# Kernel tuning notes

Hardware: AMD Instinct MI355X
Metric: run time of the kernel (lower is better)

The kernel has to match this reference:

```python
import jax, jax.numpy as jnp
import numpy as np

L = 256  # grayscale_levels
THRESH = (50.0, 150.0)
BASE = (30, 80, 150)
INCR = (10, 15, 25)


def setup_inputs() -> dict:
    key = jax.random.key(0)
    image = jax.random.uniform(key, (8, 3, 1024, 1024), dtype=jnp.float32)
    return {"image": image}


def _glcm_contrast(gray_idx):
    # gray_idx: [H, W] int32 in [0, L). distance=1, angle=0 -> horizontal neighbor pairs.
    p1 = gray_idx[:, :-1].ravel()
    p2 = gray_idx[:, 1:].ravel()
    # 256x256 co-occurrence histogram via flattened scatter-add
    hist = jnp.zeros(L * L, jnp.float32).at[p1 * L + p2].add(1.0)
    hist = hist / jnp.float32(p1.size)
    lv = jnp.arange(L, dtype=jnp.float32)
    diff2 = (lv[:, None] - lv[None, :]) ** 2
    return jnp.sum(hist.reshape(L, L) * diff2)


def _grid_labels(H, W, n_segments):
    # Deterministic grid superpixels (stand-in for skimage SLIC's initial grid;
    # same downstream math: fill each segment with its region mean).
    gr = max(1, int(round(np.sqrt(n_segments * H / W))))
    gc = max(1, int(np.ceil(n_segments / gr)))
    r = (np.arange(H) * gr) // H
    c = (np.arange(W) * gc) // W
    labels = r[:, None] * gc + c[None, :]
    return jnp.asarray(labels, dtype=jnp.int32), gr * gc


def _region_mean_saliency(gray, labels, nseg):
    flat = labels.ravel()
    sums = jax.ops.segment_sum(gray.ravel(), flat, num_segments=nseg)
    cnts = jax.ops.segment_sum(jnp.ones_like(gray).ravel(), flat, num_segments=nseg)
    return (sums / jnp.maximum(cnts, 1.0))[labels]


def reference(image):
    B, C, H, W = image.shape
    gray = 0.299 * image[:, 0] + 0.587 * image[:, 1] + 0.114 * image[:, 2]
    gidx = jnp.clip((gray * (L - 1)).astype(jnp.int32), 0, L - 1)
    complexity = jax.vmap(_glcm_contrast)(gidx)  # [B]

    comp_np = np.asarray(jax.device_get(complexity))
    cluster_sets = []
    for cv in comp_np:
        tier = 0 if cv < THRESH[0] else (1 if cv < THRESH[1] else 2)
        k, d = BASE[tier], INCR[tier]
        cluster_sets.append([k - d, k, k + d])

    # region mean uses np.mean over all channels of the region -> channel-mean image
    chan_mean = image.mean(axis=1)  # [B, H, W]
    label_cache = {}
    sal_rows = []
    for i, cset in enumerate(cluster_sets):
        maps = []
        for n in cset:
            if n not in label_cache:
                label_cache[n] = _grid_labels(H, W, n)
            labels, nseg = label_cache[n]
            maps.append(_region_mean_saliency(chan_mean[i], labels, nseg))
        sal_rows.append(jnp.stack(maps))  # [3, H, W]
    saliency = jnp.stack(sal_rows)  # [B, 3, H, W]
    return saliency, complexity, jnp.asarray(cluster_sets, dtype=jnp.int32)
```

## Files before the change

### kernel.cpp

```cpp
#include <hip/hip_runtime.h>
#include <math.h>

#define HW 1024
#define PLANE (1024 * 1024)

typedef float vf4 __attribute__((ext_vector_type(4)));

__constant__ int GCS[8]   = {5, 6, 7, 9, 10, 12, 13, 14};
__constant__ int BBASE[8] = {0, 6, 13, 21, 31, 42, 55, 69};
__constant__ int GR9c[9]      = {4, 5, 6, 8, 9, 10, 11, 12, 13};
__constant__ int GC9c[9]      = {5, 6, 7, 9, 9, 10, 12, 13, 14};
__constant__ int GBASE9c[9]   = {0, 20, 50, 92, 164, 245, 345, 477, 633};
__constant__ int COLBASE9c[9] = {0, 5, 11, 18, 18, 27, 37, 49, 62};


__device__ __forceinline__ int wave_reduce_int(int v) {
#pragma unroll
    for (int off = 32; off > 0; off >>= 1) v += __shfl_down(v, off, 64);
    return v;
}

__global__ __launch_bounds__(256) void k_main(const float* __restrict__ img,
                                              float* __restrict__ partials,
                                              float* __restrict__ rowrec) {
    const int b = blockIdx.y;
    const int tid = threadIdx.x;
    const int lane = tid & 63;
    const int w = tid >> 6;
    const int row = (blockIdx.x << 2) + w;

    const float* p = img + (size_t)b * (3 * PLANE) + row * HW;

    __shared__ float cmS[4][1024];
    __shared__ float PS[4][260];
    __shared__ float BS[4][88];
    __shared__ int swred[4];

    vf4 R[4], G[4], Bv[4];
#pragma unroll
    for (int j = 0; j < 4; ++j) {
        const int c = ((j << 6) + lane) << 2;
        R[j] = __builtin_nontemporal_load((const vf4*)(p + c));
        G[j] = __builtin_nontemporal_load((const vf4*)(p + PLANE + c));
        Bv[j] = __builtin_nontemporal_load((const vf4*)(p + 2 * PLANE + c));
    }

    int acc = 0;
    int pend = 0;
    float csum[4];

#pragma unroll
    for (int j = 0; j < 4; ++j) {
        const int c = ((j << 6) + lane) << 2;

        const float m0 = (R[j].x + G[j].x + Bv[j].x) * (1.0f / 3.0f);
        const float m1 = (R[j].y + G[j].y + Bv[j].y) * (1.0f / 3.0f);
        const float m2 = (R[j].z + G[j].z + Bv[j].z) * (1.0f / 3.0f);
        const float m3 = (R[j].w + G[j].w + Bv[j].w) * (1.0f / 3.0f);
        *(float4*)&cmS[w][c] = make_float4(m0, m1, m2, m3);
        csum[j] = (m0 + m1) + (m2 + m3);

        const float g0 = 0.299f * R[j].x + 0.587f * G[j].x + 0.114f * Bv[j].x;
        const float g1 = 0.299f * R[j].y + 0.587f * G[j].y + 0.114f * Bv[j].y;
        const float g2 = 0.299f * R[j].z + 0.587f * G[j].z + 0.114f * Bv[j].z;
        const float g3 = 0.299f * R[j].w + 0.587f * G[j].w + 0.114f * Bv[j].w;

        const int gi0 = min(max((int)(g0 * 255.0f), 0), 255);
        const int gi1 = min(max((int)(g1 * 255.0f), 0), 255);
        const int gi2 = min(max((int)(g2 * 255.0f), 0), 255);
        const int gi3 = min(max((int)(g3 * 255.0f), 0), 255);

        const int first0 = __shfl(gi0, 0, 64);
        if (j > 0 && lane == 63) {
            const int d = pend - first0;
            acc += d * d;
        }
        const int nxt = __shfl_down(gi0, 1, 64);
        const int d0 = gi0 - gi1, d1 = gi1 - gi2, d2 = gi2 - gi3;
        acc += d0 * d0 + d1 * d1 + d2 * d2;
        if (lane != 63) {
            const int d = gi3 - nxt;
            acc += d * d;
        }
        pend = gi3;
    }

    float pre = 0.0f;
#pragma unroll
    for (int j = 0; j < 4; ++j) {
        float x = csum[j];
#pragma unroll
        for (int off = 1; off < 64; off <<= 1) {
            const float y = __shfl_up(x, off, 64);
            if (lane >= off) x += y;
        }
        PS[w][(j << 6) + lane] = pre + (x - csum[j]);
        pre += __shfl(x, 63, 64);
    }
    if (lane == 0) PS[w][256] = pre;

#pragma unroll
    for (int rep = 0; rep < 2; ++rep) {
        const int bnd = lane + (rep << 6);
        if (bnd < 84) {
            const int sct = (bnd >= 6) + (bnd >= 13) + (bnd >= 21) + (bnd >= 31) +
                            (bnd >= 42) + (bnd >= 55) + (bnd >= 69);
            const int gc = GCS[sct];
            const int i = bnd - BBASE[sct];
            const int c = (i * 1024 + gc - 1) / gc;
            const int m = c & 3;
            const int cb = min(c & ~3, 1020);
            float Bp = PS[w][c >> 2];
            const float a0 = cmS[w][cb], a1 = cmS[w][cb + 1], a2 = cmS[w][cb + 2];
            if (m > 0) Bp += a0;
            if (m > 1) Bp += a1;
            if (m > 2) Bp += a2;
            BS[w][bnd] = Bp;
        }
    }

    float* rr = rowrec + (size_t)((b << 10) + row) * 80;
#pragma unroll
    for (int rep = 0; rep < 2; ++rep) {
        const int k = lane + (rep << 6);
        if (k < 76) {
            const int sct = (k >= 5) + (k >= 11) + (k >= 18) + (k >= 27) +
                            (k >= 37) + (k >= 49) + (k >= 62);
            const int bidx = k + sct;
            rr[k] = BS[w][bidx + 1] - BS[w][bidx];
        }
    }

    acc = wave_reduce_int(acc);
    if (lane == 0) swred[w] = acc;
    __syncthreads();
    if (tid == 0)
        partials[(b << 8) + blockIdx.x] = (float)(swred[0] + swred[1] + swred[2] + swred[3]);
}

__global__ __launch_bounds__(256) void k_reduce(const float* __restrict__ rowrec,
                                                const float* __restrict__ partials,
                                                float* __restrict__ cellmean,
                                                float* __restrict__ out,
                                                int* __restrict__ tier_ws) {
    const int rc = blockIdx.x, g = blockIdx.y, b = blockIdx.z;
    const int t = threadIdx.x;
    const int gr = GR9c[g];
    const bool active = (rc < gr);

    __shared__ float red[16][17];
    __shared__ float compLDS[8];

    const int gc = GC9c[g];
    const int cb = COLBASE9c[g];
    const int r0 = (rc * 1024 + gr - 1) / gr;
    const int r1 = ((rc + 1) * 1024 + gr - 1) / gr;
    const int cc = t & 15, rch = t >> 4;

    if (active) {
        float s = 0.0f;
        if (cc < gc)
            for (int r = r0 + rch; r < r1; r += 16)
                s += rowrec[(size_t)((b << 10) + r) * 80 + cb + cc];
        red[rch][cc] = s;
    }

    const bool special = (rc == 0 && g == 0 && b == 0);
    if (special) {
        const int b2 = t >> 5, sub = t & 31;
        float sC = 0.0f;
#pragma unroll
        for (int kk = 0; kk < 8; ++kk) sC += partials[(b2 << 8) + sub + (kk << 5)];
#pragma unroll
        for (int off = 16; off > 0; off >>= 1) sC += __shfl_down(sC, off, 32);
        if (sub == 0) compLDS[b2] = sC;
    }

    __syncthreads();

    if (active && rch == 0 && cc < gc) {
        float tot = 0.0f;
#pragma unroll
        for (int q = 0; q < 16; ++q) tot += red[q][cc];
        const int c0 = (cc * 1024 + gc - 1) / gc;
        const int c1 = ((cc + 1) * 1024 + gc - 1) / gc;
        const float area = (float)((r1 - r0) * (c1 - c0));
        cellmean[b * 815 + GBASE9c[g] + rc * gc + cc] = tot / area;
    }

    if (special && t < 8) {
        const size_t OFFC = (size_t)8 * 3 * PLANE;
        const float cv = compLDS[t] * (1.0f / (1024.0f * 1023.0f));
        out[OFFC + t] = cv;
        const int tier = (cv < 50.0f) ? 0 : ((cv < 150.0f) ? 1 : 2);
        const int kk = (tier == 0) ? 30 : ((tier == 1) ? 80 : 150);
        const int dd = (tier == 0) ? 10 : ((tier == 1) ? 15 : 25);
#pragma unroll
        for (int j = 0; j < 3; ++j)
            out[OFFC + 8 + t * 3 + j] = (float)(kk + (j - 1) * dd);
        tier_ws[t] = tier;
    }
}

__global__ __launch_bounds__(256) void k_fill(const int* __restrict__ tier_ws,
                                              const float* __restrict__ cellmean,
                                              float* __restrict__ out) {
    const int jm = blockIdx.y, b = blockIdx.z;
    const int tid = threadIdx.x;
    const int g = tier_ws[b] * 3 + jm;
    const int gr = GR9c[g], gc = GC9c[g];
    const float* cmb = cellmean + b * 815 + GBASE9c[g];
    float* ob = out + ((size_t)(b * 3 + jm) << 20);
    const int col = tid << 2;
    const int i0 = (col * gc) >> 10, i1 = ((col + 1) * gc) >> 10;
    const int i2 = ((col + 2) * gc) >> 10, i3 = ((col + 3) * gc) >> 10;

#pragma unroll
    for (int i = 0; i < 4; ++i) {
        const int row = (blockIdx.x << 2) + i;
        const int rc = (row * gr) >> 10;
        const float* cm = cmb + rc * gc;
        vf4 o;
        o.x = cm[i0];
        o.y = cm[i1];
        o.z = cm[i2];
        o.w = cm[i3];
        __builtin_nontemporal_store(o, (vf4*)(ob + row * HW + col));
    }
}

extern "C" void kernel_launch(void* const* d_in, const int* in_sizes, int n_in,
                              void* d_out, int out_size, void* d_ws, size_t ws_size,
                              hipStream_t stream) {
    const float* img = (const float*)d_in[0];
    float* out = (float*)d_out;
    float* ws = (float*)d_ws;

    float* partials = ws;
    int* tier_ws = (int*)(ws + 2048);
    float* cellmean = ws + 2080;
    float* rowrec = ws + 16384;

    k_main<<<dim3(256, 8), 256, 0, stream>>>(img, partials, rowrec);
    k_reduce<<<dim3(13, 9, 8), 256, 0, stream>>>(rowrec, partials, cellmean, out, tier_ws);
    k_fill<<<dim3(256, 3, 8), 256, 0, stream>>>(tier_ws, cellmean, out);
}
```

Measured before the change: 46.25 us.

## Fuse reduce and fill kernels, recomputing cell means per block in LDS

Removes the separate k_reduce launch. Each fill block now recomputes the complexity tier from partials and sums the rowrec entries for the one or two cell rows it touches, keeping the cell means in LDS before writing its output rows. This drops one kernel launch and the global round trip for cellmean and tier, at the cost of redundant partial and rowrec reads in each of the 6144 blocks plus extra barriers.

```diff
diff --git a/kernel.cpp b/kernel.cpp
--- a/kernel.cpp
+++ b/kernel.cpp
@@ -10,11 +10,15 @@
 __constant__ int BBASE[8] = {0, 6, 13, 21, 31, 42, 55, 69};
 __constant__ int GR9c[9]      = {4, 5, 6, 8, 9, 10, 11, 12, 13};
 __constant__ int GC9c[9]      = {5, 6, 7, 9, 9, 10, 12, 13, 14};
-__constant__ int GBASE9c[9]   = {0, 20, 50, 92, 164, 245, 345, 477, 633};
 __constant__ int COLBASE9c[9] = {0, 5, 11, 18, 18, 27, 37, 49, 62};
 
 
 __device__ __forceinline__ int wave_reduce_int(int v) {
+#pragma unroll
+    for (int off = 32; off > 0; off >>= 1) v += __shfl_down(v, off, 64);
+    return v;
+}
+__device__ __forceinline__ float wave_reduce_f(float v) {
 #pragma unroll
     for (int off = 32; off > 0; off >>= 1) v += __shfl_down(v, off, 64);
     return v;
@@ -138,88 +142,76 @@
         partials[(b << 8) + blockIdx.x] = (float)(swred[0] + swred[1] + swred[2] + swred[3]);
 }
 
-__global__ __launch_bounds__(256) void k_reduce(const float* __restrict__ rowrec,
-                                                const float* __restrict__ partials,
-                                                float* __restrict__ cellmean,
-                                                float* __restrict__ out,
-                                                int* __restrict__ tier_ws) {
-    const int rc = blockIdx.x, g = blockIdx.y, b = blockIdx.z;
-    const int t = threadIdx.x;
-    const int gr = GR9c[g];
-    const bool active = (rc < gr);
-
+__global__ __launch_bounds__(256) void k_fill2(const float* __restrict__ partials,
+                                               const float* __restrict__ rowrec,
+                                               float* __restrict__ out) {
+    const int rblk = blockIdx.x, jm = blockIdx.y, b = blockIdx.z;
+    const int tid = threadIdx.x;
+    const int lane = tid & 63, w = tid >> 6;
+
+    __shared__ float compLDS[4];
+    __shared__ int tierS;
     __shared__ float red[16][17];
-    __shared__ float compLDS[8];
-
-    const int gc = GC9c[g];
-    const int cb = COLBASE9c[g];
-    const int r0 = (rc * 1024 + gr - 1) / gr;
-    const int r1 = ((rc + 1) * 1024 + gr - 1) / gr;
-    const int cc = t & 15, rch = t >> 4;
-
-    if (active) {
+    __shared__ float cmLDS[2][16];
+
+    float v = partials[(b << 8) + tid];
+    v = wave_reduce_f(v);
+    if (lane == 0) compLDS[w] = v;
+    __syncthreads();
+    if (tid == 0) {
+        const float cv = (compLDS[0] + compLDS[1] + compLDS[2] + compLDS[3]) *
+                         (1.0f / (1024.0f * 1023.0f));
+        const int tier = (cv < 50.0f) ? 0 : ((cv < 150.0f) ? 1 : 2);
+        tierS = tier;
+        if (rblk == 0 && jm == 0) {
+            const size_t OFFC = (size_t)8 * 3 * PLANE;
+            out[OFFC + b] = cv;
+            const int kk = (tier == 0) ? 30 : ((tier == 1) ? 80 : 150);
+            const int dd = (tier == 0) ? 10 : ((tier == 1) ? 15 : 25);
+#pragma unroll
+            for (int j = 0; j < 3; ++j)
+                out[OFFC + 8 + b * 3 + j] = (float)(kk + (j - 1) * dd);
+        }
+    }
+    __syncthreads();
+
+    const int g = tierS * 3 + jm;
+    const int gr = GR9c[g], gc = GC9c[g], cb = COLBASE9c[g];
+    const int row0 = rblk << 2;
+    const int rc0 = (row0 * gr) >> 10;
+    const int rc3 = ((row0 + 3) * gr) >> 10;
+
+    const int cc = tid & 15, rch = tid >> 4;
+    for (int rc = rc0; rc <= rc3; ++rc) {
+        const int r0 = (rc * 1024 + gr - 1) / gr;
+        const int r1 = ((rc + 1) * 1024 + gr - 1) / gr;
         float s = 0.0f;
         if (cc < gc)
             for (int r = r0 + rch; r < r1; r += 16)
                 s += rowrec[(size_t)((b << 10) + r) * 80 + cb + cc];
         red[rch][cc] = s;
-    }
-
-    const bool special = (rc == 0 && g == 0 && b == 0);
-    if (special) {
-        const int b2 = t >> 5, sub = t & 31;
-        float sC = 0.0f;
-#pragma unroll
-        for (int kk = 0; kk < 8; ++kk) sC += partials[(b2 << 8) + sub + (kk << 5)];
-#pragma unroll
-        for (int off = 16; off > 0; off >>= 1) sC += __shfl_down(sC, off, 32);
-        if (sub == 0) compLDS[b2] = sC;
-    }
-
-    __syncthreads();
-
-    if (active && rch == 0 && cc < gc) {
-        float tot = 0.0f;
-#pragma unroll
-        for (int q = 0; q < 16; ++q) tot += red[q][cc];
-        const int c0 = (cc * 1024 + gc - 1) / gc;
-        const int c1 = ((cc + 1) * 1024 + gc - 1) / gc;
-        const float area = (float)((r1 - r0) * (c1 - c0));
-        cellmean[b * 815 + GBASE9c[g] + rc * gc + cc] = tot / area;
-    }
-
-    if (special && t < 8) {
-        const size_t OFFC = (size_t)8 * 3 * PLANE;
-        const float cv = compLDS[t] * (1.0f / (1024.0f * 1023.0f));
-        out[OFFC + t] = cv;
-        const int tier = (cv < 50.0f) ? 0 : ((cv < 150.0f) ? 1 : 2);
-        const int kk = (tier == 0) ? 30 : ((tier == 1) ? 80 : 150);
-        const int dd = (tier == 0) ? 10 : ((tier == 1) ? 15 : 25);
-#pragma unroll
-        for (int j = 0; j < 3; ++j)
-            out[OFFC + 8 + t * 3 + j] = (float)(kk + (j - 1) * dd);
-        tier_ws[t] = tier;
-    }
-}
-
-__global__ __launch_bounds__(256) void k_fill(const int* __restrict__ tier_ws,
-                                              const float* __restrict__ cellmean,
-                                              float* __restrict__ out) {
-    const int jm = blockIdx.y, b = blockIdx.z;
-    const int tid = threadIdx.x;
-    const int g = tier_ws[b] * 3 + jm;
-    const int gr = GR9c[g], gc = GC9c[g];
-    const float* cmb = cellmean + b * 815 + GBASE9c[g];
-    float* ob = out + ((size_t)(b * 3 + jm) << 20);
+        __syncthreads();
+        if (rch == 0 && cc < gc) {
+            float tot = 0.0f;
+#pragma unroll
+            for (int q = 0; q < 16; ++q) tot += red[q][cc];
+            const int c0 = (cc * 1024 + gc - 1) / gc;
+            const int c1 = ((cc + 1) * 1024 + gc - 1) / gc;
+            const float area = (float)((r1 - r0) * (c1 - c0));
+            cmLDS[rc - rc0][cc] = tot / area;
+        }
+        __syncthreads();
+    }
+
     const int col = tid << 2;
     const int i0 = (col * gc) >> 10, i1 = ((col + 1) * gc) >> 10;
     const int i2 = ((col + 2) * gc) >> 10, i3 = ((col + 3) * gc) >> 10;
-
+    float* ob = out + ((size_t)(b * 3 + jm) << 20);
 #pragma unroll
     for (int i = 0; i < 4; ++i) {
-        const int row = (blockIdx.x << 2) + i;
+        const int row = row0 + i;
         const int rc = (row * gr) >> 10;
-        const float* cm = cmb + rc * gc;
+        const float* cm = cmLDS[rc - rc0];
         vf4 o;
         o.x = cm[i0];
         o.y = cm[i1];
@@ -237,11 +229,8 @@
     float* ws = (float*)d_ws;
 
     float* partials = ws;
-    int* tier_ws = (int*)(ws + 2048);
-    float* cellmean = ws + 2080;
     float* rowrec = ws + 16384;
 
     k_main<<<dim3(256, 8), 256, 0, stream>>>(img, partials, rowrec);
-    k_reduce<<<dim3(13, 9, 8), 256, 0, stream>>>(rowrec, partials, cellmean, out, tier_ws);
-    k_fill<<<dim3(256, 3, 8), 256, 0, stream>>>(tier_ws, cellmean, out);
-}
+    k_fill2<<<dim3(256, 3, 8), 256, 0, stream>>>(partials, rowrec, out);
+}
```

New measurement: 44.81 us (median of 2 runs). -3.1%, faster.
